# Kernel tuning notes

Hardware: AMD Instinct MI355X
Metric: run time of the kernel (lower is better)

Reference implementation:

```python
import jax, jax.numpy as jnp
import numpy as np

BETA = 1.0
GAMMA = 0.25


def setup_inputs() -> dict:
    key = jax.random.key(0)
    ks = jax.random.split(key, 8)
    N, D_in, D_h, D_z = 65536, 1024, 512, 256
    s = lambda fan_in: 1.0 / np.sqrt(fan_in)
    return {
        "x": jax.random.normal(ks[0], (N, D_in), jnp.float32),
        "eW1": jax.random.normal(ks[1], (D_in, D_h), jnp.float32) * s(D_in),
        "eb1": jnp.zeros((D_h,), jnp.float32),
        "eW2": jax.random.normal(ks[2], (D_h, D_z), jnp.float32) * s(D_h),
        "eb2": jnp.zeros((D_z,), jnp.float32),
        "dW1": jax.random.normal(ks[3], (D_z, D_h), jnp.float32) * s(D_z),
        "db1": jnp.zeros((D_h,), jnp.float32),
        "dW2": jax.random.normal(ks[4], (D_h, D_in), jnp.float32) * s(D_h),
        "db2": jnp.zeros((D_in,), jnp.float32),
        "C0": jax.random.normal(ks[5], (1024, D_z), jnp.float32),
        "C1": jax.random.normal(ks[6], (512, D_z), jnp.float32),
        "C2": jax.random.normal(ks[7], (256, D_z), jnp.float32),
    }


def _nearest_idx(r, C):
    # argmin of squared euclidean distance == argmin of cdist(p=2)
    r = jax.lax.stop_gradient(r)
    d2 = jnp.sum(r * r, -1, keepdims=True) - 2.0 * (r @ C.T) + jnp.sum(C * C, -1)
    return jnp.argmin(d2, axis=-1)


def reference(x, eW1, eb1, eW2, eb2, dW1, db1, dW2, db2, C0, C1, C2):
    sg = jax.lax.stop_gradient
    # encoder: Linear -> GELU (exact) -> Linear
    z = jax.nn.gelu(x @ eW1 + eb1, approximate=False) @ eW2 + eb2
    residual = z
    output = jnp.zeros_like(z)
    losses = []
    for C in (C0, C1, C2):
        idx = _nearest_idx(residual, sg(C))
        q = C[idx]                                    # [N, 256] gather
        z2c = jnp.mean((residual - sg(q)) ** 2)       # commit input to code
        c2z = jnp.mean((sg(residual) - q) ** 2)       # move code to input
        losses.append(BETA * c2z + GAMMA * z2c)
        output = output + q
        residual = residual - q
    # straight-through: z + sg(zq) - sg(z)
    h = z + sg(output) - sg(z)
    out = jax.nn.gelu(h @ dW1 + db1, approximate=False) @ dW2 + db2
    recon_loss = jnp.mean((out - x) ** 2)
    return jnp.stack([recon_loss] + losses)  # [4]: recon, commit0, commit1, commit2
```

## Files before the change

kernel.cpp:

```cpp
#include <hip/hip_runtime.h>
#include <cstddef>


typedef __attribute__((ext_vector_type(8))) __bf16 bf16x8;
typedef __attribute__((ext_vector_type(4))) float f32x4;
typedef unsigned short u16;

__device__ __forceinline__ u16 f2bf(float f) {
    unsigned u = __float_as_uint(f);
    u += 0x7fffu + ((u >> 16) & 1u);
    return (u16)(u >> 16);
}
__device__ __forceinline__ float gelu_exact(float v) {
    return 0.5f * v * (1.0f + erff(v * 0.7071067811865475f));
}
__device__ __forceinline__ void gload16(const void* g, void* l) {
    __builtin_amdgcn_global_load_lds(
        (const __attribute__((address_space(1))) void*)g,
        (__attribute__((address_space(3))) void*)l, 16, 0, 0);
}
__device__ __forceinline__ f32x4 mfma_bf16(bf16x8 a, bf16x8 b, f32x4 c) {
    return __builtin_amdgcn_mfma_f32_16x16x32_bf16(a, b, c, 0, 0, 0);
}

__global__ __launch_bounds__(256)
void prep_weights(const float* __restrict__ eW1, const float* __restrict__ eW2,
                  const float* __restrict__ dW1, const float* __restrict__ dW2,
                  u16* __restrict__ eW1t, u16* __restrict__ eW2t,
                  u16* __restrict__ dW1t, u16* __restrict__ dW2t)
{
    const int b = blockIdx.x, t = threadIdx.x;
    if (b < 2048) {
        int e = b * 256 + t;
        int n = e >> 10, k = e & 1023;
        eW1t[e] = f2bf(eW1[(size_t)k * 512 + n]);
    } else if (b < 2560) {
        int e = (b - 2048) * 256 + t;
        int n = e >> 9, k = e & 511;
        eW2t[e] = f2bf(eW2[(size_t)k * 256 + n]);
    } else if (b < 3072) {
        int e = (b - 2560) * 256 + t;
        int n = e >> 8, k = e & 255;
        dW1t[e] = f2bf(dW1[(size_t)k * 512 + n]);
    } else {
        int e = (b - 3072) * 256 + t;
        int n = e >> 9, k = e & 511;
        dW2t[e] = f2bf(dW2[(size_t)k * 1024 + n]);
    }
}

__global__ __launch_bounds__(256)
void cb_prep(const float* __restrict__ C0, const float* __restrict__ C1,
             const float* __restrict__ C2, u16* __restrict__ Cbf,
             float* __restrict__ cnorm)
{
    __shared__ float red[256];
    const int code = blockIdx.x, t = threadIdx.x;
    const float* C;
    int local;
    if (code < 1024)      { C = C0; local = code; }
    else if (code < 1536) { C = C1; local = code - 1024; }
    else                  { C = C2; local = code - 1536; }
    const float v = C[(size_t)local * 256 + t];
    Cbf[(size_t)code * 256 + t] = f2bf(v);
    red[t] = v * v;
    __syncthreads();
    for (int s = 128; s; s >>= 1) { if (t < s) red[t] += red[t + s]; __syncthreads(); }
    if (t == 0) cnorm[code] = red[0];
}

template <int EPI, bool AF32>
__global__ __launch_bounds__(256, 2)
void gemm_mfma(const void* __restrict__ Aptr, const u16* __restrict__ Bt,
               const float* __restrict__ bias, u16* __restrict__ Obf,
               float* __restrict__ Of, const float* __restrict__ X,
               float* __restrict__ lossOut, int N, int K, int ntn,
               float lossScale)
{
    __shared__ __align__(16) u16 As[2][128 * 32];
    __shared__ __align__(16) u16 Bs[2][128 * 32];

    const int nwg = gridDim.x;
    const int bid = blockIdx.x;
    const int wg  = (bid & 7) * (nwg >> 3) + (bid >> 3);
    const int brow = (wg / ntn) * 128;
    const int bcol = (wg % ntn) * 128;

    const int t    = threadIdx.x;
    const int lane = t & 63;
    const int wid  = t >> 6;
    const int wrow = (wid >> 1) * 64, wcol = (wid & 1) * 64;
    const int lrow = lane & 15, lk8 = (lane >> 4) * 8;

    const int nt = K >> 5;

    f32x4 acc[4][4];
#pragma unroll
    for (int m = 0; m < 4; ++m)
#pragma unroll
        for (int n = 0; n < 4; ++n) acc[m][n] = (f32x4)0.f;

    const u16*   Abf = (const u16*)Aptr;
    const float* Af  = (const float*)Aptr;

    auto stageB = [&](int kt, int buf) {
#pragma unroll
        for (int it = 0; it < 2; ++it) {
            const int e0 = (it * 256 + t) * 8;
            const int row = e0 >> 5, col = e0 & 31;
            gload16(&Bt[(size_t)(bcol + row) * K + kt * 32 + col],
                    (char*)&Bs[buf][0] + (size_t)e0 * 2);
        }
    };
    auto stageA_bf = [&](int kt, int buf) {
#pragma unroll
        for (int it = 0; it < 2; ++it) {
            const int e0 = (it * 256 + t) * 8;
            const int row = e0 >> 5, col = e0 & 31;
            gload16(&Abf[(size_t)(brow + row) * K + kt * 32 + col],
                    (char*)&As[buf][0] + (size_t)e0 * 2);
        }
    };
    auto issueA_f32 = [&](int kt, float4* r) {
#pragma unroll
        for (int it = 0; it < 4; ++it) {
            const int e0 = (it * 256 + t) * 4;
            const int row = e0 >> 5, col = e0 & 31;
            r[it] = *(const float4*)&Af[(size_t)(brow + row) * K + kt * 32 + col];
        }
    };
    auto writeA_f32 = [&](int buf, const float4* r) {
#pragma unroll
        for (int it = 0; it < 4; ++it) {
            const int e0 = (it * 256 + t) * 4;
            const float4 v = r[it];
            unsigned lo = (unsigned)f2bf(v.x) | ((unsigned)f2bf(v.y) << 16);
            unsigned hi = (unsigned)f2bf(v.z) | ((unsigned)f2bf(v.w) << 16);
            *(uint2*)((char*)&As[buf][0] + (size_t)e0 * 2) = make_uint2(lo, hi);
        }
    };

    if (AF32) {
        float4 r0[4];
        issueA_f32(0, r0);
        stageB(0, 0);
        writeA_f32(0, r0);
    } else {
        stageA_bf(0, 0);
        stageB(0, 0);
    }
    __syncthreads();

    int cur = 0;
    for (int kt = 0; kt < nt; ++kt) {
        const bool last = (kt == nt - 1);
        float4 rnext[4];
        if (!last) {
            if (AF32) issueA_f32(kt + 1, rnext);
            else      stageA_bf(kt + 1, cur ^ 1);
            stageB(kt + 1, cur ^ 1);
        }
        bf16x8 a[4], b[4];
#pragma unroll
        for (int m = 0; m < 4; ++m)
            a[m] = *(const bf16x8*)&As[cur][(wrow + m * 16 + lrow) * 32 + lk8];
#pragma unroll
        for (int n = 0; n < 4; ++n)
            b[n] = *(const bf16x8*)&Bs[cur][(wcol + n * 16 + lrow) * 32 + lk8];
#pragma unroll
        for (int m = 0; m < 4; ++m)
#pragma unroll
            for (int n = 0; n < 4; ++n)
                acc[m][n] = mfma_bf16(a[m], b[n], acc[m][n]);

        if (AF32 && !last) writeA_f32(cur ^ 1, rnext);
        __syncthreads();
        cur ^= 1;
    }

    int   colN[4];
    float bn[4];
#pragma unroll
    for (int n = 0; n < 4; ++n) {
        colN[n] = bcol + wcol + n * 16 + lrow;
        bn[n]   = bias[colN[n]];
    }

    if (EPI == 0) {
#pragma unroll
        for (int m = 0; m < 4; ++m) {
            const int rowb = brow + wrow + m * 16 + (lane >> 4) * 4;
#pragma unroll
            for (int n = 0; n < 4; ++n)
#pragma unroll
                for (int j = 0; j < 4; ++j)
                    Obf[(size_t)(rowb + j) * N + colN[n]] =
                        f2bf(gelu_exact(acc[m][n][j] + bn[n]));
        }
    } else if (EPI == 1) {
#pragma unroll
        for (int m = 0; m < 4; ++m) {
            const int rowb = brow + wrow + m * 16 + (lane >> 4) * 4;
#pragma unroll
            for (int n = 0; n < 4; ++n)
#pragma unroll
                for (int j = 0; j < 4; ++j)
                    Of[(size_t)(rowb + j) * N + colN[n]] = acc[m][n][j] + bn[n];
        }
    } else {
        float partial = 0.f;
#pragma unroll
        for (int m = 0; m < 4; ++m) {
            const int rowb = brow + wrow + m * 16 + (lane >> 4) * 4;
#pragma unroll
            for (int n = 0; n < 4; ++n)
#pragma unroll
                for (int j = 0; j < 4; ++j) {
                    const float o = acc[m][n][j] + bn[n];
                    const float d = o - X[(size_t)(rowb + j) * N + colN[n]];
                    partial = fmaf(d, d, partial);
                }
        }
        float* red = (float*)&As[0][0];
        red[t] = partial;
        __syncthreads();
        for (int s = 128; s; s >>= 1) { if (t < s) red[t] += red[t + s]; __syncthreads(); }
        if (t == 0) atomicAdd(lossOut, red[0] * lossScale);
    }
}

__global__ __launch_bounds__(512, 4)
void vq_mfma(const float* __restrict__ Z, const u16* __restrict__ Cbf,
             const float* __restrict__ cnorm,
             const float* __restrict__ C0, const float* __restrict__ C1,
             const float* __restrict__ C2,
             u16* __restrict__ ZQ, float* __restrict__ lossOut)
{
    __shared__ __align__(16) u16 Rb[64][264];
    __shared__ __align__(16) u16 Cs[2][32 * 256];
    __shared__ float redv[64][2];
    __shared__ int   redi[64][2];
    __shared__ int   idxs[3][64];
    __shared__ float lred[8];

    const int t    = threadIdx.x;
    const int lane = t & 63;
    const int wid  = t >> 6;
    const int rg   = wid & 3;
    const int cg   = wid >> 2;
    const int lrow = lane & 15, g = lane >> 4;
    const int col  = t & 255;
    const int rh   = t >> 8;
    const int brow = blockIdx.x * 64;

    float R[32];
#pragma unroll
    for (int r = 0; r < 32; ++r)
        R[r] = Z[(size_t)(brow + rh * 32 + r) * 256 + col];

    const float* Cf[3]  = {C0, C1, C2};
    const int ncodes[3] = {1024, 512, 256};
    const int coff[3]   = {0, 1024, 1536};
    const float lscale  = 1.25f / (65536.0f * 256.0f);

    for (int stage = 0; stage < 3; ++stage) {
        const u16*   Cb  = Cbf + (size_t)coff[stage] * 256;
        const float* cns = cnorm + coff[stage];
        const int ntile  = ncodes[stage] >> 5;

        auto stageC = [&](int tile, int buf) {
#pragma unroll
            for (int it = 0; it < 2; ++it) {
                const int d   = (it * 512 + t) * 16;
                const int row = d >> 9;
                const int kb  = d & 511;
                const int kbs = kb ^ ((row & 7) << 4);
                gload16(&Cb[(size_t)(tile * 32 + row) * 256 + (kbs >> 1)],
                        (char*)&Cs[buf][0] + d);
            }
        };

        stageC(0, 0);
#pragma unroll
        for (int r = 0; r < 32; ++r) Rb[rh * 32 + r][col] = f2bf(R[r]);
        __syncthreads();

        bf16x8 a[8];
#pragma unroll
        for (int ks = 0; ks < 8; ++ks)
            a[ks] = *(const bf16x8*)&Rb[rg * 16 + lrow][ks * 32 + g * 8];

        float best[4]; int bidx[4];
#pragma unroll
        for (int j = 0; j < 4; ++j) { best[j] = 3.0e38f; bidx[j] = 0; }

        const int cr = cg * 16 + lrow;

        int buf = 0;
#pragma unroll 1
        for (int tile = 0; tile < ntile; ++tile) {
            if (tile + 1 < ntile) stageC(tile + 1, buf ^ 1);
            const int   code = tile * 32 + cr;
            const float cn   = cns[code];
            f32x4 acc = (f32x4)0.f;
#pragma unroll
            for (int ks = 0; ks < 8; ++ks) {
                const int kb = (ks * 64 + g * 16) ^ ((cr & 7) << 4);
                bf16x8 b = *(const bf16x8*)((const char*)&Cs[buf][0]
                             + cr * 512 + kb);
                acc = mfma_bf16(a[ks], b, acc);
            }
#pragma unroll
            for (int j = 0; j < 4; ++j) {
                const float s = fmaf(-2.0f, acc[j], cn);
                if (s < best[j]) { best[j] = s; bidx[j] = code; }
            }
            __syncthreads();
            buf ^= 1;
        }

#pragma unroll
        for (int j = 0; j < 4; ++j) {
            float v = best[j]; int i = bidx[j];
#pragma unroll
            for (int d = 1; d < 16; d <<= 1) {
                const float ov = __shfl_xor(v, d);
                const int   oi = __shfl_xor(i, d);
                if (ov < v || (ov == v && oi < i)) { v = ov; i = oi; }
            }
            if (lrow == 0) {
                redv[rg * 16 + g * 4 + j][cg] = v;
                redi[rg * 16 + g * 4 + j][cg] = i;
            }
        }
        __syncthreads();
        if (t < 64) {
            float v = redv[t][0]; int i = redi[t][0];
            const float ov = redv[t][1]; const int oi = redi[t][1];
            if (ov < v || (ov == v && oi < i)) { v = ov; i = oi; }
            idxs[stage][t] = i;
        }
        __syncthreads();

        const float* Cfs = Cf[stage];
        float partial = 0.f;
#pragma unroll
        for (int r = 0; r < 32; ++r) {
            const float q  = Cfs[(size_t)idxs[stage][rh * 32 + r] * 256 + col];
            const float rn = R[r] - q;
            R[r] = rn;
            partial = fmaf(rn, rn, partial);
        }
#pragma unroll
        for (int d = 32; d; d >>= 1) partial += __shfl_down(partial, d);
        if (lane == 0) lred[wid] = partial;
        __syncthreads();
        if (t == 0) {
            float s = 0.f;
#pragma unroll
            for (int w2 = 0; w2 < 8; ++w2) s += lred[w2];
            atomicAdd(&lossOut[1 + stage], s * lscale);
        }
        __syncthreads();
    }

#pragma unroll
    for (int r = 0; r < 32; ++r) {
        const int row = rh * 32 + r;
        const float zq = C0[(size_t)idxs[0][row] * 256 + col]
                       + C1[(size_t)idxs[1][row] * 256 + col]
                       + C2[(size_t)idxs[2][row] * 256 + col];
        ZQ[(size_t)(brow + row) * 256 + col] = f2bf(zq);
    }
}

extern "C" void kernel_launch(void* const* d_in, const int* in_sizes, int n_in,
                              void* d_out, int out_size, void* d_ws, size_t ws_size,
                              hipStream_t stream)
{
    const float* x   = (const float*)d_in[0];
    const float* eW1 = (const float*)d_in[1];
    const float* eb1 = (const float*)d_in[2];
    const float* eW2 = (const float*)d_in[3];
    const float* eb2 = (const float*)d_in[4];
    const float* dW1 = (const float*)d_in[5];
    const float* db1 = (const float*)d_in[6];
    const float* dW2 = (const float*)d_in[7];
    const float* db2 = (const float*)d_in[8];
    const float* C0  = (const float*)d_in[9];
    const float* C1  = (const float*)d_in[10];
    const float* C2  = (const float*)d_in[11];
    float* out = (float*)d_out;

    char* w = (char*)d_ws;
    u16*   H1   = (u16*)(w);
    float* Zf   = (float*)(w + ((size_t)64 << 20));
    u16*   ZQ   = (u16*)(w + ((size_t)128 << 20));
    u16*   H2   = (u16*)(w + ((size_t)160 << 20));
    u16*   eW1t = (u16*)(w + ((size_t)224 << 20));
    u16*   eW2t = (u16*)(w + ((size_t)225 << 20));
    u16*   dW1t = (u16*)(w + ((size_t)226 << 20));
    u16*   dW2t = (u16*)(w + ((size_t)227 << 20));
    u16*   Cbf  = (u16*)(w + ((size_t)228 << 20));
    float* cn   = (float*)(w + ((size_t)229 << 20));

    hipMemsetAsync(d_out, 0, 4 * sizeof(float), stream);

    prep_weights<<<5120, 256, 0, stream>>>(eW1, eW2, dW1, dW2, eW1t, eW2t, dW1t, dW2t);
    cb_prep<<<1792, 256, 0, stream>>>(C0, C1, C2, Cbf, cn);

    gemm_mfma<0, true><<<2048, 256, 0, stream>>>(
        x, eW1t, eb1, H1, nullptr, nullptr, nullptr, 512, 1024, 4, 0.f);
    gemm_mfma<1, false><<<1024, 256, 0, stream>>>(
        H1, eW2t, eb2, nullptr, Zf, nullptr, nullptr, 256, 512, 2, 0.f);
    vq_mfma<<<1024, 512, 0, stream>>>(Zf, Cbf, cn, C0, C1, C2, ZQ, out);
    gemm_mfma<0, false><<<2048, 256, 0, stream>>>(
        ZQ, dW1t, db1, H2, nullptr, nullptr, nullptr, 512, 256, 4, 0.f);
    gemm_mfma<2, false><<<4096, 256, 0, stream>>>(
        H2, dW2t, db2, nullptr, nullptr, x, out, 1024, 512, 8,
        1.0f / (65536.0f * 1024.0f));
}
```

Measured before the change: 545.3 us.

## Pre-convert x to bf16, widen GEMM K-tile to 64 with XOR-swizzled LDS

Adds a prep kernel that converts x to bf16 once. Both the first encoder GEMM (A operand) and the reconstruction-loss epilogue then read the half-size copy instead of fp32 with in-loop conversion. The GEMM K tile grows from 32 to 64, and LDS uses an XOR-swizzled layout loaded with global_load_lds for both operands, to halve the barrier count and avoid bank conflicts. This costs an extra pass over x (read 256MB, write 128MB) and doubles the LDS footprint. The loss also now compares against bf16-rounded x, which slightly changes precision.

```diff
diff --git a/kernel.cpp b/kernel.cpp
--- a/kernel.cpp
+++ b/kernel.cpp
@@ -11,6 +11,9 @@
     u += 0x7fffu + ((u >> 16) & 1u);
     return (u16)(u >> 16);
 }
+__device__ __forceinline__ float bf2f(u16 b) {
+    return __uint_as_float((unsigned)b << 16);
+}
 __device__ __forceinline__ float gelu_exact(float v) {
     return 0.5f * v * (1.0f + erff(v * 0.7071067811865475f));
 }
@@ -21,6 +24,23 @@
 }
 __device__ __forceinline__ f32x4 mfma_bf16(bf16x8 a, bf16x8 b, f32x4 c) {
     return __builtin_amdgcn_mfma_f32_16x16x32_bf16(a, b, c, 0, 0, 0);
+}
+
+__global__ __launch_bounds__(256)
+void prep_x(const float* __restrict__ x, u16* __restrict__ xbf)
+{
+    const size_t total = (size_t)65536 * 1024;
+    const size_t step  = (size_t)gridDim.x * 256 * 8;
+    for (size_t i = ((size_t)blockIdx.x * 256 + threadIdx.x) * 8; i < total; i += step) {
+        float4 v0 = *(const float4*)&x[i];
+        float4 v1 = *(const float4*)&x[i + 4];
+        uint4 o;
+        o.x = (unsigned)f2bf(v0.x) | ((unsigned)f2bf(v0.y) << 16);
+        o.y = (unsigned)f2bf(v0.z) | ((unsigned)f2bf(v0.w) << 16);
+        o.z = (unsigned)f2bf(v1.x) | ((unsigned)f2bf(v1.y) << 16);
+        o.w = (unsigned)f2bf(v1.z) | ((unsigned)f2bf(v1.w) << 16);
+        *(uint4*)&xbf[i] = o;
+    }
 }
 
 __global__ __launch_bounds__(256)
@@ -69,16 +89,16 @@
     if (t == 0) cnorm[code] = red[0];
 }
 
-template <int EPI, bool AF32>
+template <int EPI>
 __global__ __launch_bounds__(256, 2)
-void gemm_mfma(const void* __restrict__ Aptr, const u16* __restrict__ Bt,
+void gemm_mfma(const u16* __restrict__ A, const u16* __restrict__ Bt,
                const float* __restrict__ bias, u16* __restrict__ Obf,
-               float* __restrict__ Of, const float* __restrict__ X,
+               float* __restrict__ Of, const u16* __restrict__ Xbf,
                float* __restrict__ lossOut, int N, int K, int ntn,
                float lossScale)
 {
-    __shared__ __align__(16) u16 As[2][128 * 32];
-    __shared__ __align__(16) u16 Bs[2][128 * 32];
+    __shared__ __align__(16) u16 As[2][128 * 64];
+    __shared__ __align__(16) u16 Bs[2][128 * 64];
 
     const int nwg = gridDim.x;
     const int bid = blockIdx.x;
@@ -90,9 +110,9 @@
     const int lane = t & 63;
     const int wid  = t >> 6;
     const int wrow = (wid >> 1) * 64, wcol = (wid & 1) * 64;
-    const int lrow = lane & 15, lk8 = (lane >> 4) * 8;
-
-    const int nt = K >> 5;
+    const int lrow = lane & 15, g = lane >> 4;
+
+    const int nt = K >> 6;
 
     f32x4 acc[4][4];
 #pragma unroll
@@ -100,80 +120,49 @@
 #pragma unroll
         for (int n = 0; n < 4; ++n) acc[m][n] = (f32x4)0.f;
 
-    const u16*   Abf = (const u16*)Aptr;
-    const float* Af  = (const float*)Aptr;
-
-    auto stageB = [&](int kt, int buf) {
-#pragma unroll
-        for (int it = 0; it < 2; ++it) {
-            const int e0 = (it * 256 + t) * 8;
-            const int row = e0 >> 5, col = e0 & 31;
-            gload16(&Bt[(size_t)(bcol + row) * K + kt * 32 + col],
-                    (char*)&Bs[buf][0] + (size_t)e0 * 2);
+    auto stage = [&](const u16* __restrict__ src, int row0, int kt, u16* dst) {
+#pragma unroll
+        for (int it = 0; it < 4; ++it) {
+            const int d   = (it * 256 + t) * 16;
+            const int row = d >> 7;
+            const int ch  = (d >> 4) & 7;
+            const int cs  = ch ^ (row & 7);
+            gload16(&src[(size_t)(row0 + row) * K + kt * 64 + cs * 8],
+                    (char*)dst + d);
         }
     };
-    auto stageA_bf = [&](int kt, int buf) {
-#pragma unroll
-        for (int it = 0; it < 2; ++it) {
-            const int e0 = (it * 256 + t) * 8;
-            const int row = e0 >> 5, col = e0 & 31;
-            gload16(&Abf[(size_t)(brow + row) * K + kt * 32 + col],
-                    (char*)&As[buf][0] + (size_t)e0 * 2);
-        }
-    };
-    auto issueA_f32 = [&](int kt, float4* r) {
-#pragma unroll
-        for (int it = 0; it < 4; ++it) {
-            const int e0 = (it * 256 + t) * 4;
-            const int row = e0 >> 5, col = e0 & 31;
-            r[it] = *(const float4*)&Af[(size_t)(brow + row) * K + kt * 32 + col];
-        }
-    };
-    auto writeA_f32 = [&](int buf, const float4* r) {
-#pragma unroll
-        for (int it = 0; it < 4; ++it) {
-            const int e0 = (it * 256 + t) * 4;
-            const float4 v = r[it];
-            unsigned lo = (unsigned)f2bf(v.x) | ((unsigned)f2bf(v.y) << 16);
-            unsigned hi = (unsigned)f2bf(v.z) | ((unsigned)f2bf(v.w) << 16);
-            *(uint2*)((char*)&As[buf][0] + (size_t)e0 * 2) = make_uint2(lo, hi);
-        }
-    };
-
-    if (AF32) {
-        float4 r0[4];
-        issueA_f32(0, r0);
-        stageB(0, 0);
-        writeA_f32(0, r0);
-    } else {
-        stageA_bf(0, 0);
-        stageB(0, 0);
-    }
+
+    stage(A, brow, 0, As[0]);
+    stage(Bt, bcol, 0, Bs[0]);
     __syncthreads();
 
     int cur = 0;
     for (int kt = 0; kt < nt; ++kt) {
-        const bool last = (kt == nt - 1);
-        float4 rnext[4];
-        if (!last) {
-            if (AF32) issueA_f32(kt + 1, rnext);
-            else      stageA_bf(kt + 1, cur ^ 1);
-            stageB(kt + 1, cur ^ 1);
-        }
-        bf16x8 a[4], b[4];
-#pragma unroll
-        for (int m = 0; m < 4; ++m)
-            a[m] = *(const bf16x8*)&As[cur][(wrow + m * 16 + lrow) * 32 + lk8];
-#pragma unroll
-        for (int n = 0; n < 4; ++n)
-            b[n] = *(const bf16x8*)&Bs[cur][(wcol + n * 16 + lrow) * 32 + lk8];
-#pragma unroll
-        for (int m = 0; m < 4; ++m)
-#pragma unroll
-            for (int n = 0; n < 4; ++n)
-                acc[m][n] = mfma_bf16(a[m], b[n], acc[m][n]);
-
-        if (AF32 && !last) writeA_f32(cur ^ 1, rnext);
+        if (kt + 1 < nt) {
+            stage(A, brow, kt + 1, As[cur ^ 1]);
+            stage(Bt, bcol, kt + 1, Bs[cur ^ 1]);
+        }
+#pragma unroll
+        for (int ks = 0; ks < 2; ++ks) {
+            bf16x8 a[4], b[4];
+#pragma unroll
+            for (int m = 0; m < 4; ++m) {
+                const int R = wrow + m * 16 + lrow;
+                a[m] = *(const bf16x8*)((const char*)&As[cur][0]
+                         + R * 128 + (((ks * 4 + g) ^ (R & 7)) << 4));
+            }
+#pragma unroll
+            for (int n = 0; n < 4; ++n) {
+                const int R = wcol + n * 16 + lrow;
+                b[n] = *(const bf16x8*)((const char*)&Bs[cur][0]
+                         + R * 128 + (((ks * 4 + g) ^ (R & 7)) << 4));
+            }
+#pragma unroll
+            for (int m = 0; m < 4; ++m)
+#pragma unroll
+                for (int n = 0; n < 4; ++n)
+                    acc[m][n] = mfma_bf16(a[m], b[n], acc[m][n]);
+        }
         __syncthreads();
         cur ^= 1;
     }
@@ -217,7 +206,7 @@
 #pragma unroll
                 for (int j = 0; j < 4; ++j) {
                     const float o = acc[m][n][j] + bn[n];
-                    const float d = o - X[(size_t)(rowb + j) * N + colN[n]];
+                    const float d = o - bf2f(Xbf[(size_t)(rowb + j) * N + colN[n]]);
                     partial = fmaf(d, d, partial);
                 }
         }
@@ -397,6 +386,7 @@
     float* Zf   = (float*)(w + ((size_t)64 << 20));
     u16*   ZQ   = (u16*)(w + ((size_t)128 << 20));
     u16*   H2   = (u16*)(w + ((size_t)160 << 20));
+    u16*   xbf  = (u16*)(w + ((size_t)230 << 20));
     u16*   eW1t = (u16*)(w + ((size_t)224 << 20));
     u16*   eW2t = (u16*)(w + ((size_t)225 << 20));
     u16*   dW1t = (u16*)(w + ((size_t)226 << 20));
@@ -406,17 +396,18 @@
 
     hipMemsetAsync(d_out, 0, 4 * sizeof(float), stream);
 
+    prep_x<<<4096, 256, 0, stream>>>(x, xbf);
     prep_weights<<<5120, 256, 0, stream>>>(eW1, eW2, dW1, dW2, eW1t, eW2t, dW1t, dW2t);
     cb_prep<<<1792, 256, 0, stream>>>(C0, C1, C2, Cbf, cn);
 
-    gemm_mfma<0, true><<<2048, 256, 0, stream>>>(
-        x, eW1t, eb1, H1, nullptr, nullptr, nullptr, 512, 1024, 4, 0.f);
-    gemm_mfma<1, false><<<1024, 256, 0, stream>>>(
+    gemm_mfma<0><<<2048, 256, 0, stream>>>(
+        xbf, eW1t, eb1, H1, nullptr, nullptr, nullptr, 512, 1024, 4, 0.f);
+    gemm_mfma<1><<<1024, 256, 0, stream>>>(
         H1, eW2t, eb2, nullptr, Zf, nullptr, nullptr, 256, 512, 2, 0.f);
     vq_mfma<<<1024, 512, 0, stream>>>(Zf, Cbf, cn, C0, C1, C2, ZQ, out);
-    gemm_mfma<0, false><<<2048, 256, 0, stream>>>(
+    gemm_mfma<0><<<2048, 256, 0, stream>>>(
         ZQ, dW1t, db1, H2, nullptr, nullptr, nullptr, 512, 256, 4, 0.f);
-    gemm_mfma<2, false><<<4096, 256, 0, stream>>>(
-        H2, dW2t, db2, nullptr, nullptr, x, out, 1024, 512, 8,
+    gemm_mfma<2><<<4096, 256, 0, stream>>>(
+        H2, dW2t, db2, nullptr, nullptr, xbf, out, 1024, 512, 8,
         1.0f / (65536.0f * 1024.0f));
 }
```

Result: slower. 557.2 us (+2.2%).
